# Performance work log

Measured on AMD Instinct MI355X. Metric: run time of the kernel, lower is better.

The kernel has to match this reference:

```python
import jax, jax.numpy as jnp
import numpy as np

EPS = 1e-4      # MovingBatchNorm eps
STEPS = 3       # fixed RK4 steps standing in for adaptive dopri5
B, N, D, C, H = 4, 2048, 3, 64, 512


def setup_inputs() -> dict:
    key = jax.random.key(0)
    ks = iter(jax.random.split(key, 40))
    f32 = jnp.float32

    def rn(shape, s=1.0):
        return jax.random.normal(next(ks), shape, dtype=f32) * s

    inp = {}
    inp['x'] = rn((B, N, D))
    inp['c'] = rn((B, N, C))
    for p in ('bn1', 'bn2'):
        inp[p + '_mean'] = rn((D,), 0.1)
        inp[p + '_var'] = jax.random.uniform(next(ks), (D,), dtype=f32, minval=0.5, maxval=1.5)
        inp[p + '_log_gamma'] = jnp.zeros((D,), f32)
        inp[p + '_beta'] = jnp.zeros((D,), f32)
    inp['sqrt_T'] = jnp.array([np.sqrt(0.5)], f32)  # train_T: T = sqrt_T**2
    dims = [(D, H), (H, H), (H, H), (H, D)]  # concatsquash (in, out)
    for i, (din, dout) in enumerate(dims):
        inp[f'W{i}'] = rn((dout, din), 0.05)
        inp[f'b{i}'] = jnp.zeros((dout,), f32)
        inp[f'Wg{i}'] = rn((dout, C + 1), 0.05)
        inp[f'bg{i}'] = jnp.zeros((dout,), f32)
        inp[f'Wb{i}'] = rn((dout, C + 1), 0.05)
    return inp


def _odenet(t, x, c, layers):
    # ConcatSquash MLP: lin(x)*sigmoid(hyper_gate([t,c])) + hyper_bias([t,c])
    ctx = jnp.concatenate([jnp.broadcast_to(t, c.shape[:-1] + (1,)).astype(x.dtype), c], axis=-1)
    h = x
    for i, (W, b, Wg, bg, Wb) in enumerate(layers):
        h = (h @ W.T + b) * jax.nn.sigmoid(ctx @ Wg.T + bg) + ctx @ Wb.T
        if i < len(layers) - 1:
            h = jnp.tanh(h)
    return h


def _aug_dyn(t, x, c, layers):
    # augmented CNF dynamics: (dx/dt, dlogp/dt) with exact divergence via D jvps
    f = lambda xx: _odenet(t, xx, c, layers)
    div = jnp.zeros(x.shape[:-1] + (1,), x.dtype)
    dx = None
    for i in range(x.shape[-1]):
        e = jnp.zeros_like(x).at[..., i].set(1.0)
        dx, jv = jax.jvp(f, (x,), (e,))
        div = div + jv[..., i:i + 1]
    return dx, -div


def _rk4(x0, lp0, c, layers, T):
    dt = T / STEPS

    def step(carry, i):
        x, lp = carry
        t = i.astype(x.dtype) * dt
        k1x, k1l = _aug_dyn(t, x, c, layers)
        k2x, k2l = _aug_dyn(t + 0.5 * dt, x + 0.5 * dt * k1x, c, layers)
        k3x, k3l = _aug_dyn(t + 0.5 * dt, x + 0.5 * dt * k2x, c, layers)
        k4x, k4l = _aug_dyn(t + dt, x + dt * k3x, c, layers)
        x = x + (dt / 6.0) * (k1x + 2.0 * k2x + 2.0 * k3x + k4x)
        lp = lp + (dt / 6.0) * (k1l + 2.0 * k2l + 2.0 * k3l + k4l)
        return (x, lp), None

    (x, lp), _ = jax.lax.scan(step, (x0, lp0), jnp.arange(STEPS))
    return x, lp


def _bn(x, lp, mean, var, log_gamma, beta):
    # MovingBatchNorm1d, eval mode; logdet = sum(log_gamma - 0.5*log(var+eps))
    y = (x - mean) * jnp.exp(log_gamma) / jnp.sqrt(var + EPS) + beta
    ld = jnp.sum(log_gamma - 0.5 * jnp.log(var + EPS))
    return y, lp - ld


def reference(x, c, bn1_mean, bn1_var, bn1_log_gamma, bn1_beta,
              bn2_mean, bn2_var, bn2_log_gamma, bn2_beta, sqrt_T,
              W0, b0, Wg0, bg0, Wb0, W1, b1, Wg1, bg1, Wb1,
              W2, b2, Wg2, bg2, Wb2, W3, b3, Wg3, bg3, Wb3):
    layers = [(W0, b0, Wg0, bg0, Wb0), (W1, b1, Wg1, bg1, Wb1),
              (W2, b2, Wg2, bg2, Wb2), (W3, b3, Wg3, bg3, Wb3)]
    lp = jnp.zeros(x.shape[:-1] + (1,), x.dtype)  # (B,N,1)
    x, lp = _bn(x, lp, bn1_mean, bn1_var, bn1_log_gamma, bn1_beta)
    T = sqrt_T[0] ** 2
    x, lp = _rk4(x, lp, c, layers, T)
    x, lp = _bn(x, lp, bn2_mean, bn2_var, bn2_log_gamma, bn2_beta)
    return x, jnp.sum(lp, axis=(1, 2))
```

## Files before the change

### kernel.cpp

```cpp
#include <hip/hip_runtime.h>
#include <hip/hip_fp8.h>

#define PTS 8192
#define HDIM 512
#define BN_EPS 1e-4f
#define HSTRB 528
#define TS 256.0f
#define SCL1 0x7f7f7f7f

typedef unsigned short u16;
typedef unsigned char u8;
typedef long long i64;
typedef u16 u16x8 __attribute__((ext_vector_type(8)));
typedef short s16x8 __attribute__((ext_vector_type(8)));
typedef float f32x4 __attribute__((ext_vector_type(4)));
typedef float f32x2 __attribute__((ext_vector_type(2)));
typedef int i32x4 __attribute__((ext_vector_type(4)));
typedef int i32x8 __attribute__((ext_vector_type(8)));

__device__ __forceinline__ float bf2f(u16 u) {
  unsigned x = ((unsigned)u) << 16;
  return __builtin_bit_cast(float, x);
}
__device__ __forceinline__ u16 f2bf(float f) {
  unsigned x = __builtin_bit_cast(unsigned, f);
  x += 0x7fffu + ((x >> 16) & 1u);
  return (u16)(x >> 16);
}
__device__ __forceinline__ u8 f2f8(float x) {
  int v = __builtin_amdgcn_cvt_pk_fp8_f32(x, x, 0, false);
  return (u8)(v & 0xff);
}
__device__ __forceinline__ unsigned pk4_f8(float a, float b, float c, float d) {
  int v = __builtin_amdgcn_cvt_pk_fp8_f32(a, b, 0, false);
  v = __builtin_amdgcn_cvt_pk_fp8_f32(c, d, v, true);
  return (unsigned)v;
}
__device__ __forceinline__ float sigf(float x) {
  return __builtin_amdgcn_rcpf(1.f + __expf(-x));
}
__device__ __forceinline__ float fast_tanh(float x) {
  float e = __expf(2.f * x);
  return 1.f - 2.f * __builtin_amdgcn_rcpf(e + 1.f);
}
__device__ __forceinline__ void gl2lds16(const u16* g, u16* l) {
  __builtin_amdgcn_global_load_lds(
      (const __attribute__((address_space(1))) void*)g,
      (__attribute__((address_space(3))) void*)l, 16, 0, 0);
}
__device__ __forceinline__ i32x8 ld32(const u8* p) {
  i32x4 lo = *(const i32x4*)p;
  i32x4 hi = *(const i32x4*)(p + 16);
  return __builtin_shufflevector(lo, hi, 0, 1, 2, 3, 4, 5, 6, 7);
}

#define MFMA_SC(A, B, C) \
  __builtin_amdgcn_mfma_scale_f32_16x16x128_f8f6f4((A), (B), (C), 0, 0, 0, SCL1, 0, SCL1)

#define MX_GEMM(WL)                                                         \
  {                                                                         \
    _Pragma("unroll")                                                       \
    for (int zi = 0; zi < 4; ++zi)                                          \
      _Pragma("unroll")                                                     \
      for (int zj = 0; zj < 4; ++zj)                                        \
        _Pragma("unroll")                                                   \
        for (int zr = 0; zr < 4; ++zr) acc[zi][zj][zr] = 0.f;               \
    const u8* wp = (WL);                                                    \
    _Pragma("unroll 1")                                                     \
    for (int c = 0; c < 4; ++c) {                                           \
      const u8* hc = hb + c * 128;                                          \
      i32x8 af0 = ld32(hc);                                                 \
      i32x8 af1 = ld32(hc + (size_t)16 * HSTRB);                            \
      i32x8 af2 = ld32(hc + (size_t)32 * HSTRB);                            \
      i32x8 af3 = ld32(hc + (size_t)48 * HSTRB);                            \
      i32x8 bA = ld32(wp);                                                  \
      i32x8 bB = ld32(wp + 2048);                                           \
      __builtin_amdgcn_sched_barrier(0);                                    \
      __builtin_amdgcn_s_setprio(1);                                        \
      acc[0][0] = MFMA_SC(af0, bA, acc[0][0]);                              \
      acc[1][0] = MFMA_SC(af1, bA, acc[1][0]);                              \
      acc[2][0] = MFMA_SC(af2, bA, acc[2][0]);                              \
      acc[3][0] = MFMA_SC(af3, bA, acc[3][0]);                              \
      acc[0][1] = MFMA_SC(af0, bB, acc[0][1]);                              \
      acc[1][1] = MFMA_SC(af1, bB, acc[1][1]);                              \
      acc[2][1] = MFMA_SC(af2, bB, acc[2][1]);                              \
      acc[3][1] = MFMA_SC(af3, bB, acc[3][1]);                              \
      __builtin_amdgcn_s_setprio(0);                                        \
      __builtin_amdgcn_sched_barrier(0);                                    \
      bA = ld32(wp + 4096);                                                 \
      bB = ld32(wp + 6144);                                                 \
      __builtin_amdgcn_sched_barrier(0);                                    \
      __builtin_amdgcn_s_setprio(1);                                        \
      acc[0][2] = MFMA_SC(af0, bA, acc[0][2]);                              \
      acc[1][2] = MFMA_SC(af1, bA, acc[1][2]);                              \
      acc[2][2] = MFMA_SC(af2, bA, acc[2][2]);                              \
      acc[3][2] = MFMA_SC(af3, bA, acc[3][2]);                              \
      acc[0][3] = MFMA_SC(af0, bB, acc[0][3]);                              \
      acc[1][3] = MFMA_SC(af1, bB, acc[1][3]);                              \
      acc[2][3] = MFMA_SC(af2, bB, acc[2][3]);                              \
      acc[3][3] = MFMA_SC(af3, bB, acc[3][3]);                              \
      __builtin_amdgcn_s_setprio(0);                                        \
      __builtin_amdgcn_sched_barrier(0);                                    \
      wp += 65536;                                                          \
    }                                                                       \
  }

struct PrepArgs {
  const float *W1, *W2;
  u8 *W1s, *W2s;
  const float* c;
  u16* cb;
  const float *Wg0, *Wg1, *Wg2, *Wb0, *Wb1, *Wb2;
  const float *bg0, *bg1, *bg2;
  u16* Wpack;
  float* bias_pack;
  const float *x, *m1, *v1, *lg1, *be1;
  float *x_cur;
  const float *Wg3, *bg3, *Wb3;
  float *G3, *B3;
  const float *W0, *b0, *b1, *b2, *W3;
  float *E0, *E1, *E2;
};
__global__ void prep_kernel(PrepArgs a) {
  int i = blockIdx.x * 256 + threadIdx.x;
  if (i < 512 * 512) {
    int n = i >> 9, k = i & 511;
    int c = k >> 7, q2 = (k >> 5) & 3, b = k & 31;
    int w = n >> 6, j = (n >> 4) & 3, lr = n & 15;
    size_t d = (size_t)c * 65536 + (size_t)w * 8192 + (size_t)j * 2048 +
               (size_t)(q2 * 16 + lr) * 32 + b;
    a.W1s[d] = f2f8(a.W1[i]);
    a.W2s[d] = f2f8(a.W2[i]);
  }
  if (i < PTS * 64) a.cb[i] = f2bf(a.c[i]);
  if (i < 6 * 512 * 64) {
    int sec = i >> 15;
    int within = i & 32767;
    int o = within >> 6, k = within & 63;
    const float* src[6] = {a.Wg0, a.Wg1, a.Wg2, a.Wb0, a.Wb1, a.Wb2};
    a.Wpack[i] = f2bf(src[sec][o * 65 + 1 + k]);
  }
  if (i < 3072) {
    int sec = i >> 9, o = i & 511;
    const float* bgl[3] = {a.bg0, a.bg1, a.bg2};
    a.bias_pack[i] = (sec < 3) ? bgl[sec][o] : 0.f;
  }
  if (i < 512) {
    int o = i;
    a.E0[o * 8 + 0] = a.W0[o * 3];
    a.E0[o * 8 + 1] = a.W0[o * 3 + 1];
    a.E0[o * 8 + 2] = a.W0[o * 3 + 2];
    a.E0[o * 8 + 3] = a.b0[o];
    a.E0[o * 8 + 4] = a.Wg0[o * 65];
    a.E0[o * 8 + 5] = a.Wb0[o * 65];
    a.E0[o * 8 + 6] = 0.f; a.E0[o * 8 + 7] = 0.f;
    a.E1[o * 4 + 0] = a.b1[o];
    a.E1[o * 4 + 1] = a.Wg1[o * 65];
    a.E1[o * 4 + 2] = a.Wb1[o * 65];
    a.E1[o * 4 + 3] = 0.f;
    a.E2[o * 8 + 0] = a.b2[o];
    a.E2[o * 8 + 1] = a.Wg2[o * 65];
    a.E2[o * 8 + 2] = a.Wb2[o * 65];
    a.E2[o * 8 + 3] = a.W3[o];
    a.E2[o * 8 + 4] = a.W3[512 + o];
    a.E2[o * 8 + 5] = a.W3[1024 + o];
    a.E2[o * 8 + 6] = 0.f; a.E2[o * 8 + 7] = 0.f;
  }
  if (i < PTS * 3) {
    int d = i % 3;
    a.x_cur[i] = (a.x[i] - a.m1[d]) * __expf(a.lg1[d]) * rsqrtf(a.v1[d] + BN_EPS) + a.be1[d];
  }
  {
    int lane = threadIdx.x & 63;
    int p = (blockIdx.x * 256 + threadIdx.x) >> 6;
    float cv = a.c[(size_t)p * 64 + lane];
    float ag[3], ab[3];
    #pragma unroll
    for (int o = 0; o < 3; ++o) {
      ag[o] = cv * a.Wg3[o * 65 + 1 + lane];
      ab[o] = cv * a.Wb3[o * 65 + 1 + lane];
    }
    #pragma unroll
    for (int off = 32; off > 0; off >>= 1) {
      #pragma unroll
      for (int o = 0; o < 3; ++o) {
        ag[o] += __shfl_xor(ag[o], off);
        ab[o] += __shfl_xor(ab[o], off);
      }
    }
    if (lane == 0) {
      #pragma unroll
      for (int o = 0; o < 3; ++o) {
        a.G3[p * 3 + o] = ag[o] + a.bg3[o];
        a.B3[p * 3 + o] = ab[o];
      }
    }
  }
}

struct GatesGemmArgs {
  const u16 *A, *W;
  const float* bias;
  u16* GBi;
};
__global__ __launch_bounds__(256) void gates_gemm(GatesGemmArgs a) {
  __shared__ u16 As[128 * 32];
  __shared__ u16 Bs[128 * 32];
  int tid = threadIdx.x;
  int m0 = blockIdx.x * 128, n0 = blockIdx.y * 128;
  int wave = tid >> 6, lane = tid & 63;
  int wm = (wave & 1) * 64, wn = (wave >> 1) * 64;
  int lr = lane & 15, quad = lane >> 4;

  int rowS = tid >> 2, colS = (tid & 3) * 8;
  const u16* gA0 = a.A + (size_t)(m0 + rowS) * 64 + colS;
  const u16* gB0 = a.W + (size_t)(n0 + rowS) * 64 + colS;
  u16* sA0 = &As[tid * 8];
  u16* sA1 = &As[2048 + tid * 8];
  u16* sB0 = &Bs[tid * 8];
  u16* sB1 = &Bs[2048 + tid * 8];

  f32x4 acc[4][4];
  #pragma unroll
  for (int i = 0; i < 4; ++i)
    #pragma unroll
    for (int j = 0; j < 4; ++j)
      #pragma unroll
      for (int r = 0; r < 4; ++r) acc[i][j][r] = 0.f;

  for (int k0 = 0; k0 < 64; k0 += 32) {
    if (k0) __syncthreads();
    gl2lds16(gA0 + k0, sA0);
    gl2lds16(gA0 + (size_t)64 * 64 + k0, sA1);
    gl2lds16(gB0 + k0, sB0);
    gl2lds16(gB0 + (size_t)64 * 64 + k0, sB1);
    __syncthreads();
    s16x8 af[4], bfr[4];
    #pragma unroll
    for (int i = 0; i < 4; ++i)
      af[i] = *(const s16x8*)&As[(wm + i * 16 + lr) * 32 + quad * 8];
    #pragma unroll
    for (int j = 0; j < 4; ++j)
      bfr[j] = *(const s16x8*)&Bs[(wn + j * 16 + lr) * 32 + quad * 8];
    #pragma unroll
    for (int i = 0; i < 4; ++i)
      #pragma unroll
      for (int j = 0; j < 4; ++j)
        acc[i][j] = __builtin_amdgcn_mfma_f32_16x16x32_bf16(af[i], bfr[j], acc[i][j], 0, 0, 0);
  }

  #pragma unroll
  for (int j = 0; j < 4; ++j) {
    int n = n0 + wn + j * 16 + lr;
    int sec = n >> 9, col = n & 511;
    int l = (sec < 3) ? sec : sec - 3;
    int off = col * 2 + ((sec < 3) ? 0 : 1);
    float bv = a.bias[n];
    u16* outp = a.GBi + (size_t)l * PTS * 1024 + off;
    #pragma unroll
    for (int i = 0; i < 4; ++i) {
      int mrow = m0 + wm + i * 16 + quad * 4;
      #pragma unroll
      for (int r = 0; r < 4; ++r)
        outp[(size_t)(mrow + r) * 1024] = f2bf(acc[i][j][r] + bv);
    }
  }
}

struct FlowArgs {
  const float* sqrtT;
  const float *G3, *B3, *Wg3, *Wb3, *b3;
  const float* x0;
  const u16 *GBi0, *GBi1, *GBi2;
  const float *E0, *E1, *E2;
  const u8 *W1s, *W2s;
  const float *m2, *v2, *lg2, *be2;
  float* out_x;
  float* lp_state;
};

__global__ __launch_bounds__(512, 4) void flow_kernel(FlowArgs a) {
  __shared__ __align__(16) u8 Hs[64 * HSTRB];
  __shared__ float xe[16][3];
  __shared__ float part[8][16][6];
  __shared__ float xs[16][3], kxs[16][3];
  __shared__ float kls[16], lps[16];
  __shared__ float g3s[16][3], b3s[16][3];

  int tid = threadIdx.x;
  int w = tid >> 6, lane = tid & 63, lr = lane & 15, quad = lane >> 4;
  int n0 = w * 64;
  int p0 = blockIdx.x * 16;
  float s0 = a.sqrtT[0];
  float dt = s0 * s0 * (1.f / 3.f);

  const u8* w1l = a.W1s + (size_t)w * 8192 + (size_t)lane * 32;
  const u8* w2l = a.W2s + (size_t)w * 8192 + (size_t)lane * 32;
  const u8* hb = (const u8*)Hs + (size_t)lr * HSTRB + quad * 32;

  float wg3r[3], wb3r[3], b3r[3];
  #pragma unroll
  for (int r = 0; r < 3; ++r) {
    wg3r[r] = a.Wg3[r * 65];
    wb3r[r] = a.Wb3[r * 65];
    b3r[r] = a.b3[r];
  }

  if (tid < 16) {
    int p = p0 + tid;
    #pragma unroll
    for (int r = 0; r < 3; ++r) {
      xs[tid][r] = a.x0[p * 3 + r];
      g3s[tid][r] = a.G3[p * 3 + r];
      b3s[tid][r] = a.B3[p * 3 + r];
    }
    lps[tid] = 0.f;
  }

  int pl0 = tid >> 5;
  int base_o = (tid & 31) * 16;
  const u16* g0row = a.GBi0 + (size_t)(p0 + pl0) * 1024 + 2 * base_o;

  #pragma unroll 1
  for (int s = 0; s < 12; ++s) {
    int sub = s & 3;
    float ts_cur = (float)(s >> 2) + ((sub == 0) ? 0.f : (sub == 3) ? 1.f : 0.5f);

    u16x8 gc0 = *(const u16x8*)(g0row);
    u16x8 gc1 = *(const u16x8*)(g0row + 8);
    u16x8 gc2 = *(const u16x8*)(g0row + 16);
    u16x8 gc3 = *(const u16x8*)(g0row + 24);

    __syncthreads();

    if (tid < 16) {
      float o0 = xs[tid][0], o1 = xs[tid][1], o2 = xs[tid][2];
      if (s > 0) {
        int m = (s - 1) & 3;
        float ts_prev = (float)((s - 1) >> 2) + ((m == 0) ? 0.f : (m == 3) ? 1.f : 0.5f);
        float tp = ts_prev * dt;
        float fr[6];
        #pragma unroll
        for (int r = 0; r < 6; ++r) {
          float sum = part[0][tid][r];
          #pragma unroll
          for (int ww = 1; ww < 8; ++ww) sum += part[ww][tid][r];
          fr[r] = sum;
        }
        float dx[3], gate[3];
        #pragma unroll
        for (int r = 0; r < 3; ++r) {
          gate[r] = sigf(g3s[tid][r] + tp * wg3r[r]);
          float bias = b3s[tid][r] + tp * wb3r[r];
          dx[r] = fmaf(fr[r] + b3r[r], gate[r], bias);
        }
        float klv = -(fr[3] * gate[0] + fr[4] * gate[1] + fr[5] * gate[2]);
        if (m == 0) {
          o0 += 0.5f * dt * dx[0]; o1 += 0.5f * dt * dx[1]; o2 += 0.5f * dt * dx[2];
          kxs[tid][0] = dx[0]; kxs[tid][1] = dx[1]; kxs[tid][2] = dx[2];
          kls[tid] = klv;
        } else if (m == 1) {
          o0 += 0.5f * dt * dx[0]; o1 += 0.5f * dt * dx[1]; o2 += 0.5f * dt * dx[2];
          kxs[tid][0] += 2.f * dx[0]; kxs[tid][1] += 2.f * dx[1]; kxs[tid][2] += 2.f * dx[2];
          kls[tid] += 2.f * klv;
        } else if (m == 2) {
          o0 += dt * dx[0]; o1 += dt * dx[1]; o2 += dt * dx[2];
          kxs[tid][0] += 2.f * dx[0]; kxs[tid][1] += 2.f * dx[1]; kxs[tid][2] += 2.f * dx[2];
          kls[tid] += 2.f * klv;
        } else {
          float sc = dt * (1.f / 6.f);
          o0 = xs[tid][0] + sc * (kxs[tid][0] + dx[0]);
          o1 = xs[tid][1] + sc * (kxs[tid][1] + dx[1]);
          o2 = xs[tid][2] + sc * (kxs[tid][2] + dx[2]);
          xs[tid][0] = o0; xs[tid][1] = o1; xs[tid][2] = o2;
          lps[tid] += sc * (kls[tid] + klv);
        }
      }
      xe[tid][0] = o0; xe[tid][1] = o1; xe[tid][2] = o2;
    }
    __syncthreads();

    float t = ts_cur * dt;

    {
      float x0v = xe[pl0][0], x1v = xe[pl0][1], x2v = xe[pl0][2];
      u16x8 gcv[4] = {gc0, gc1, gc2, gc3};
      #pragma unroll
      for (int cc = 0; cc < 4; ++cc) {
        u16x8 v = gcv[cc];
        float hk[4], d0k[4], d1k[4], d2k[4];
        #pragma unroll
        for (int k = 0; k < 4; ++k) {
          int o = base_o + cc * 4 + k;
          f32x4 e = *(const f32x4*)(a.E0 + (size_t)o * 8);
          f32x2 e2 = *(const f32x2*)(a.E0 + (size_t)o * 8 + 4);
          float u = fmaf(e[0], x0v, fmaf(e[1], x1v, e[2] * x2v)) + e[3];
          float gate = sigf(bf2f(v[2 * k]) + t * e2[0]);
          float bias = bf2f(v[2 * k + 1]) + t * e2[1];
          float z = fmaf(u, gate, bias);
          float h = fast_tanh(z);
          float wm = (1.f - h * h) * gate * TS;
          hk[k] = h;
          d0k[k] = wm * e[0];
          d1k[k] = wm * e[1];
          d2k[k] = wm * e[2];
        }
        size_t hbb = (size_t)(pl0 * 4) * HSTRB + base_o + cc * 4;
        *(unsigned*)(Hs + hbb) = pk4_f8(hk[0], hk[1], hk[2], hk[3]);
        *(unsigned*)(Hs + hbb + HSTRB) = pk4_f8(d0k[0], d0k[1], d0k[2], d0k[3]);
        *(unsigned*)(Hs + hbb + 2 * HSTRB) = pk4_f8(d1k[0], d1k[1], d1k[2], d1k[3]);
        *(unsigned*)(Hs + hbb + 3 * HSTRB) = pk4_f8(d2k[0], d2k[1], d2k[2], d2k[3]);
      }
    }
    __syncthreads();

    f32x4 acc[4][4];
    MX_GEMM(w1l)

    unsigned g1v[4][4];
    #pragma unroll
    for (int j = 0; j < 4; ++j)
      #pragma unroll
      for (int i = 0; i < 4; ++i)
        g1v[j][i] = *(const unsigned*)(a.GBi1 + (size_t)(p0 + i * 4 + quad) * 1024 +
                                       2 * (n0 + j * 16 + lr));

    __syncthreads();

    #pragma unroll
    for (int j = 0; j < 4; ++j) {
      int n = n0 + j * 16 + lr;
      f32x4 e1 = *(const f32x4*)(a.E1 + (size_t)n * 4);
      #pragma unroll
      for (int i = 0; i < 4; ++i) {
        unsigned d = g1v[j][i];
        float gate = sigf(bf2f((u16)(d & 0xffffu)) + t * e1[1]);
        float bias = bf2f((u16)(d >> 16)) + t * e1[2];
        f32x4 u = acc[i][j];
        float z = fmaf(u[0] + e1[0], gate, bias);
        float h = fast_tanh(z);
        float wmf = (1.f - h * h) * gate;
        int row = i * 16 + quad * 4;
        Hs[(size_t)row * HSTRB + n] = f2f8(h);
        Hs[(size_t)(row + 1) * HSTRB + n] = f2f8(u[1] * wmf);
        Hs[(size_t)(row + 2) * HSTRB + n] = f2f8(u[2] * wmf);
        Hs[(size_t)(row + 3) * HSTRB + n] = f2f8(u[3] * wmf);
      }
    }
    __syncthreads();

    MX_GEMM(w2l)

    unsigned g2v[4][4];
    #pragma unroll
    for (int j = 0; j < 4; ++j)
      #pragma unroll
      for (int i = 0; i < 4; ++i)
        g2v[j][i] = *(const unsigned*)(a.GBi2 + (size_t)(p0 + i * 4 + quad) * 1024 +
                                       2 * (n0 + j * 16 + lr));

    #pragma unroll
    for (int i = 0; i < 4; ++i) {
      float v0 = 0.f, v1 = 0.f, v2 = 0.f, v3 = 0.f, v4 = 0.f, v5 = 0.f;
      int pl = i * 4 + quad;
      #pragma unroll
      for (int j = 0; j < 4; ++j) {
        int n = n0 + j * 16 + lr;
        f32x4 ea = *(const f32x4*)(a.E2 + (size_t)n * 8);
        f32x2 eb = *(const f32x2*)(a.E2 + (size_t)n * 8 + 4);
        unsigned d = g2v[j][i];
        float gate = sigf(bf2f((u16)(d & 0xffffu)) + t * ea[1]);
        float bias = bf2f((u16)(d >> 16)) + t * ea[2];
        f32x4 u = acc[i][j];
        float z = fmaf(u[0] + ea[0], gate, bias);
        float h = fast_tanh(z);
        float wmf = (1.f - h * h) * gate;
        float w30 = ea[3], w31 = eb[0], w32 = eb[1];
        v0 = fmaf(h, w30, v0);
        v1 = fmaf(h, w31, v1);
        v2 = fmaf(h, w32, v2);
        v3 = fmaf(u[1] * wmf, w30, v3);
        v4 = fmaf(u[2] * wmf, w31, v4);
        v5 = fmaf(u[3] * wmf, w32, v5);
      }
      #pragma unroll
      for (int mask = 1; mask <= 8; mask <<= 1) {
        v0 += __shfl_xor(v0, mask);
        v1 += __shfl_xor(v1, mask);
        v2 += __shfl_xor(v2, mask);
        v3 += __shfl_xor(v3, mask);
        v4 += __shfl_xor(v4, mask);
        v5 += __shfl_xor(v5, mask);
      }
      float val = (lr == 0) ? v0 : (lr == 1) ? v1 : (lr == 2) ? v2
                : (lr == 3) ? v3 * (1.f / TS) : (lr == 4) ? v4 * (1.f / TS)
                : v5 * (1.f / TS);
      if (lr < 6) part[w][pl][lr] = val;
    }
  }

  __syncthreads();

  if (tid < 16) {
    int p = p0 + tid;
    float tp = 3.f * dt;
    float fr[6];
    #pragma unroll
    for (int r = 0; r < 6; ++r) {
      float sum = part[0][tid][r];
      #pragma unroll
      for (int ww = 1; ww < 8; ++ww) sum += part[ww][tid][r];
      fr[r] = sum;
    }
    float dx[3], gate[3];
    #pragma unroll
    for (int r = 0; r < 3; ++r) {
      gate[r] = sigf(g3s[tid][r] + tp * wg3r[r]);
      float bias = b3s[tid][r] + tp * wb3r[r];
      dx[r] = fmaf(fr[r] + b3r[r], gate[r], bias);
    }
    float klv = -(fr[3] * gate[0] + fr[4] * gate[1] + fr[5] * gate[2]);
    float sc = dt * (1.f / 6.f);
    #pragma unroll
    for (int r = 0; r < 3; ++r) {
      float xf = xs[tid][r] + sc * (kxs[tid][r] + dx[r]);
      a.out_x[p * 3 + r] =
          (xf - a.m2[r]) * __expf(a.lg2[r]) * rsqrtf(a.v2[r] + BN_EPS) + a.be2[r];
    }
    a.lp_state[p] = lps[tid] + sc * (kls[tid] + klv);
  }
}

__global__ void finish_lp(const float* __restrict__ lp_state,
                          const float* __restrict__ v1, const float* __restrict__ lg1,
                          const float* __restrict__ v2, const float* __restrict__ lg2,
                          float* __restrict__ out) {
  int b = blockIdx.x, tid = threadIdx.x;
  float s = 0.f;
  for (int n = tid; n < 2048; n += 256) s += lp_state[b * 2048 + n];
  __shared__ float red[256];
  red[tid] = s;
  __syncthreads();
  for (int w = 128; w > 0; w >>= 1) {
    if (tid < w) red[tid] += red[tid + w];
    __syncthreads();
  }
  if (tid == 0) {
    float ld = 0.f;
    for (int d = 0; d < 3; ++d) {
      ld += lg1[d] - 0.5f * logf(v1[d] + BN_EPS);
      ld += lg2[d] - 0.5f * logf(v2[d] + BN_EPS);
    }
    out[b] = red[0] - 2048.f * ld;
  }
}

extern "C" void kernel_launch(void* const* d_in, const int* in_sizes, int n_in,
                              void* d_out, int out_size, void* d_ws, size_t ws_size,
                              hipStream_t stream) {
  const float* x        = (const float*)d_in[0];
  const float* c        = (const float*)d_in[1];
  const float* bn1_mean = (const float*)d_in[2];
  const float* bn1_var  = (const float*)d_in[3];
  const float* bn1_lg   = (const float*)d_in[4];
  const float* bn1_beta = (const float*)d_in[5];
  const float* bn2_mean = (const float*)d_in[6];
  const float* bn2_var  = (const float*)d_in[7];
  const float* bn2_lg   = (const float*)d_in[8];
  const float* bn2_beta = (const float*)d_in[9];
  const float* sqrtT    = (const float*)d_in[10];
  const float* W0  = (const float*)d_in[11];
  const float* b0  = (const float*)d_in[12];
  const float* Wg0 = (const float*)d_in[13];
  const float* bg0 = (const float*)d_in[14];
  const float* Wb0 = (const float*)d_in[15];
  const float* W1  = (const float*)d_in[16];
  const float* b1  = (const float*)d_in[17];
  const float* Wg1 = (const float*)d_in[18];
  const float* bg1 = (const float*)d_in[19];
  const float* Wb1 = (const float*)d_in[20];
  const float* W2  = (const float*)d_in[21];
  const float* b2  = (const float*)d_in[22];
  const float* Wg2 = (const float*)d_in[23];
  const float* bg2 = (const float*)d_in[24];
  const float* Wb2 = (const float*)d_in[25];
  const float* W3  = (const float*)d_in[26];
  const float* b3  = (const float*)d_in[27];
  const float* Wg3 = (const float*)d_in[28];
  const float* bg3 = (const float*)d_in[29];
  const float* Wb3 = (const float*)d_in[30];

  char* base = (char*)d_ws;
  size_t off = 0;
  auto alloc = [&](size_t bytes) -> void* {
    void* pp = base + off;
    off += (bytes + 255) & ~(size_t)255;
    return pp;
  };
  u8* W1s = (u8*)alloc((size_t)512 * 512);
  u8* W2s = (u8*)alloc((size_t)512 * 512);
  u16* cb  = (u16*)alloc((size_t)PTS * 64 * 2);
  u16* Wpack = (u16*)alloc((size_t)6 * 512 * 64 * 2);
  float* bias_pack = (float*)alloc((size_t)3072 * 4);
  u16* GBi = (u16*)alloc((size_t)3 * PTS * 1024 * 2);
  const size_t SZi = (size_t)PTS * 1024;
  u16* GBi0 = GBi;
  u16* GBi1 = GBi + SZi;
  u16* GBi2 = GBi + 2 * SZi;
  float* G3f = (float*)alloc((size_t)PTS * 3 * 4);
  float* B3f = (float*)alloc((size_t)PTS * 3 * 4);
  float* E0 = (float*)alloc((size_t)512 * 8 * 4);
  float* E1 = (float*)alloc((size_t)512 * 4 * 4);
  float* E2 = (float*)alloc((size_t)512 * 8 * 4);
  float* x_cur    = (float*)alloc((size_t)PTS * 3 * 4);
  float* lp_state = (float*)alloc((size_t)PTS * 4);
  (void)ws_size; (void)in_sizes; (void)n_in; (void)out_size;

  PrepArgs pa{W1, W2, W1s, W2s, c, cb, Wg0, Wg1, Wg2, Wb0, Wb1, Wb2,
              bg0, bg1, bg2, Wpack, bias_pack, x, bn1_mean, bn1_var,
              bn1_lg, bn1_beta, x_cur, Wg3, bg3, Wb3, G3f, B3f,
              W0, b0, b1, b2, W3, E0, E1, E2};
  prep_kernel<<<2048, 256, 0, stream>>>(pa);

  GatesGemmArgs gg{cb, Wpack, bias_pack, GBi};
  gates_gemm<<<dim3(64, 24), 256, 0, stream>>>(gg);

  FlowArgs fa{sqrtT, G3f, B3f, Wg3, Wb3, b3, x_cur, GBi0, GBi1, GBi2,
              E0, E1, E2, W1s, W2s, bn2_mean, bn2_var, bn2_lg, bn2_beta,
              (float*)d_out, lp_state};
  flow_kernel<<<PTS / 16, 512, 0, stream>>>(fa);

  finish_lp<<<4, 256, 0, stream>>>(lp_state, bn1_var, bn1_lg, bn2_var, bn2_lg,
                                   (float*)d_out + PTS * 3);
}
```

Baseline: 563.8 us.

## Double-buffer hidden LDS and compute RK state redundantly to drop barriers

Splits the shared hidden-activation buffer into two (one per GEMM layer), so the barrier between the first GEMM and the layer-2 activation writes can be removed. The per-substep RK4 state update, previously done by 16 threads and broadcast through shared memory behind an extra barrier, is now recomputed by every thread for its own point. Only one designated thread per point writes the shared state, and the x state is double-buffered by step parity. It also prefetches next-substep layer-0 gate/bias loads and hoists pointer arithmetic for the gate loads. This trades more LDS and redundant ALU work for two fewer block-wide barriers per substep.

```diff
diff --git a/kernel.cpp b/kernel.cpp
--- a/kernel.cpp
+++ b/kernel.cpp
@@ -57,7 +57,7 @@
 #define MFMA_SC(A, B, C) \
   __builtin_amdgcn_mfma_scale_f32_16x16x128_f8f6f4((A), (B), (C), 0, 0, 0, SCL1, 0, SCL1)
 
-#define MX_GEMM(WL)                                                         \
+#define MX_GEMM(WL, HB)                                                     \
   {                                                                         \
     _Pragma("unroll")                                                       \
     for (int zi = 0; zi < 4; ++zi)                                          \
@@ -68,7 +68,7 @@
     const u8* wp = (WL);                                                    \
     _Pragma("unroll 1")                                                     \
     for (int c = 0; c < 4; ++c) {                                           \
-      const u8* hc = hb + c * 128;                                          \
+      const u8* hc = (HB) + c * 128;                                        \
       i32x8 af0 = ld32(hc);                                                 \
       i32x8 af1 = ld32(hc + (size_t)16 * HSTRB);                            \
       i32x8 af2 = ld32(hc + (size_t)32 * HSTRB);                            \
@@ -280,10 +280,10 @@
 };
 
 __global__ __launch_bounds__(512, 4) void flow_kernel(FlowArgs a) {
-  __shared__ __align__(16) u8 Hs[64 * HSTRB];
-  __shared__ float xe[16][3];
-  __shared__ float part[8][16][6];
-  __shared__ float xs[16][3], kxs[16][3];
+  __shared__ __align__(16) u8 HsA[64 * HSTRB];
+  __shared__ __align__(16) u8 HsB[64 * HSTRB];
+  __shared__ float part[8][16][8];
+  __shared__ float xs[2][16][3], kxs[16][3];
   __shared__ float kls[16], lps[16];
   __shared__ float g3s[16][3], b3s[16][3];
 
@@ -291,12 +291,16 @@
   int w = tid >> 6, lane = tid & 63, lr = lane & 15, quad = lane >> 4;
   int n0 = w * 64;
   int p0 = blockIdx.x * 16;
+  int pl0 = tid >> 5;
+  int base_o = (tid & 31) * 16;
+  bool desig = (tid & 31) == 0;
   float s0 = a.sqrtT[0];
   float dt = s0 * s0 * (1.f / 3.f);
 
   const u8* w1l = a.W1s + (size_t)w * 8192 + (size_t)lane * 32;
   const u8* w2l = a.W2s + (size_t)w * 8192 + (size_t)lane * 32;
-  const u8* hb = (const u8*)Hs + (size_t)lr * HSTRB + quad * 32;
+  const u8* hbA = (const u8*)HsA + (size_t)lr * HSTRB + quad * 32;
+  const u8* hbB = (const u8*)HsB + (size_t)lr * HSTRB + quad * 32;
 
   float wg3r[3], wb3r[3], b3r[3];
   #pragma unroll
@@ -306,84 +310,83 @@
     b3r[r] = a.b3[r];
   }
 
-  if (tid < 16) {
-    int p = p0 + tid;
+  const u16* g0p = a.GBi0 + (size_t)(p0 + pl0) * 1024 + 2 * base_o;
+  const u16* g1p = a.GBi1 + (size_t)(p0 + quad) * 1024 + 2 * (n0 + lr);
+  const u16* g2p = a.GBi2 + (size_t)(p0 + quad) * 1024 + 2 * (n0 + lr);
+
+  if (desig) {
     #pragma unroll
     for (int r = 0; r < 3; ++r) {
-      xs[tid][r] = a.x0[p * 3 + r];
-      g3s[tid][r] = a.G3[p * 3 + r];
-      b3s[tid][r] = a.B3[p * 3 + r];
-    }
-    lps[tid] = 0.f;
-  }
-
-  int pl0 = tid >> 5;
-  int base_o = (tid & 31) * 16;
-  const u16* g0row = a.GBi0 + (size_t)(p0 + pl0) * 1024 + 2 * base_o;
+      xs[0][pl0][r] = a.x0[(p0 + pl0) * 3 + r];
+      g3s[pl0][r] = a.G3[(p0 + pl0) * 3 + r];
+      b3s[pl0][r] = a.B3[(p0 + pl0) * 3 + r];
+    }
+    lps[pl0] = 0.f;
+  }
+  u16x8 gc0 = *(const u16x8*)(g0p);
+  u16x8 gc1 = *(const u16x8*)(g0p + 8);
+  u16x8 gc2 = *(const u16x8*)(g0p + 16);
+  u16x8 gc3 = *(const u16x8*)(g0p + 24);
+  __syncthreads();
 
   #pragma unroll 1
   for (int s = 0; s < 12; ++s) {
     int sub = s & 3;
-    float ts_cur = (float)(s >> 2) + ((sub == 0) ? 0.f : (sub == 3) ? 1.f : 0.5f);
-
-    u16x8 gc0 = *(const u16x8*)(g0row);
-    u16x8 gc1 = *(const u16x8*)(g0row + 8);
-    u16x8 gc2 = *(const u16x8*)(g0row + 16);
-    u16x8 gc3 = *(const u16x8*)(g0row + 24);
-
-    __syncthreads();
-
-    if (tid < 16) {
-      float o0 = xs[tid][0], o1 = xs[tid][1], o2 = xs[tid][2];
-      if (s > 0) {
-        int m = (s - 1) & 3;
-        float ts_prev = (float)((s - 1) >> 2) + ((m == 0) ? 0.f : (m == 3) ? 1.f : 0.5f);
-        float tp = ts_prev * dt;
-        float fr[6];
-        #pragma unroll
-        for (int r = 0; r < 6; ++r) {
-          float sum = part[0][tid][r];
-          #pragma unroll
-          for (int ww = 1; ww < 8; ++ww) sum += part[ww][tid][r];
-          fr[r] = sum;
+    float t = ((float)(s >> 2) + ((sub == 0) ? 0.f : (sub == 3) ? 1.f : 0.5f)) * dt;
+
+    float o0, o1, o2;
+    if (s == 0) {
+      o0 = xs[0][pl0][0]; o1 = xs[0][pl0][1]; o2 = xs[0][pl0][2];
+    } else {
+      int m = (s - 1) & 3, q = (s - 1) >> 2;
+      float tp = ((float)q + ((m == 0) ? 0.f : (m == 3) ? 1.f : 0.5f)) * dt;
+      float fr0 = 0.f, fr1 = 0.f, fr2 = 0.f, fr3 = 0.f, fr4 = 0.f, fr5 = 0.f;
+      #pragma unroll
+      for (int ww = 0; ww < 8; ++ww) {
+        f32x4 pa = *(const f32x4*)&part[ww][pl0][0];
+        f32x2 pb = *(const f32x2*)&part[ww][pl0][4];
+        fr0 += pa[0]; fr1 += pa[1]; fr2 += pa[2];
+        fr3 += pa[3]; fr4 += pb[0]; fr5 += pb[1];
+      }
+      float ga0 = sigf(g3s[pl0][0] + tp * wg3r[0]);
+      float ga1 = sigf(g3s[pl0][1] + tp * wg3r[1]);
+      float ga2 = sigf(g3s[pl0][2] + tp * wg3r[2]);
+      float dx0 = fmaf(fr0 + b3r[0], ga0, b3s[pl0][0] + tp * wb3r[0]);
+      float dx1 = fmaf(fr1 + b3r[1], ga1, b3s[pl0][1] + tp * wb3r[1]);
+      float dx2 = fmaf(fr2 + b3r[2], ga2, b3s[pl0][2] + tp * wb3r[2]);
+      float klv = -(fr3 * ga0 + fr4 * ga1 + fr5 * ga2);
+      float bx0 = xs[q & 1][pl0][0];
+      float bx1 = xs[q & 1][pl0][1];
+      float bx2 = xs[q & 1][pl0][2];
+      if (m == 3) {
+        float sc = dt * (1.f / 6.f);
+        o0 = bx0 + sc * (kxs[pl0][0] + dx0);
+        o1 = bx1 + sc * (kxs[pl0][1] + dx1);
+        o2 = bx2 + sc * (kxs[pl0][2] + dx2);
+        if (desig) {
+          xs[(q + 1) & 1][pl0][0] = o0;
+          xs[(q + 1) & 1][pl0][1] = o1;
+          xs[(q + 1) & 1][pl0][2] = o2;
+          lps[pl0] += sc * (kls[pl0] + klv);
         }
-        float dx[3], gate[3];
-        #pragma unroll
-        for (int r = 0; r < 3; ++r) {
-          gate[r] = sigf(g3s[tid][r] + tp * wg3r[r]);
-          float bias = b3s[tid][r] + tp * wb3r[r];
-          dx[r] = fmaf(fr[r] + b3r[r], gate[r], bias);
+      } else {
+        float cf = (m == 2) ? dt : 0.5f * dt;
+        o0 = fmaf(cf, dx0, bx0);
+        o1 = fmaf(cf, dx1, bx1);
+        o2 = fmaf(cf, dx2, bx2);
+        if (desig) {
+          if (m == 0) {
+            kxs[pl0][0] = dx0; kxs[pl0][1] = dx1; kxs[pl0][2] = dx2;
+            kls[pl0] = klv;
+          } else {
+            kxs[pl0][0] += 2.f * dx0; kxs[pl0][1] += 2.f * dx1; kxs[pl0][2] += 2.f * dx2;
+            kls[pl0] += 2.f * klv;
+          }
         }
-        float klv = -(fr[3] * gate[0] + fr[4] * gate[1] + fr[5] * gate[2]);
-        if (m == 0) {
-          o0 += 0.5f * dt * dx[0]; o1 += 0.5f * dt * dx[1]; o2 += 0.5f * dt * dx[2];
-          kxs[tid][0] = dx[0]; kxs[tid][1] = dx[1]; kxs[tid][2] = dx[2];
-          kls[tid] = klv;
-        } else if (m == 1) {
-          o0 += 0.5f * dt * dx[0]; o1 += 0.5f * dt * dx[1]; o2 += 0.5f * dt * dx[2];
-          kxs[tid][0] += 2.f * dx[0]; kxs[tid][1] += 2.f * dx[1]; kxs[tid][2] += 2.f * dx[2];
-          kls[tid] += 2.f * klv;
-        } else if (m == 2) {
-          o0 += dt * dx[0]; o1 += dt * dx[1]; o2 += dt * dx[2];
-          kxs[tid][0] += 2.f * dx[0]; kxs[tid][1] += 2.f * dx[1]; kxs[tid][2] += 2.f * dx[2];
-          kls[tid] += 2.f * klv;
-        } else {
-          float sc = dt * (1.f / 6.f);
-          o0 = xs[tid][0] + sc * (kxs[tid][0] + dx[0]);
-          o1 = xs[tid][1] + sc * (kxs[tid][1] + dx[1]);
-          o2 = xs[tid][2] + sc * (kxs[tid][2] + dx[2]);
-          xs[tid][0] = o0; xs[tid][1] = o1; xs[tid][2] = o2;
-          lps[tid] += sc * (kls[tid] + klv);
-        }
-      }
-      xe[tid][0] = o0; xe[tid][1] = o1; xe[tid][2] = o2;
-    }
-    __syncthreads();
-
-    float t = ts_cur * dt;
+      }
+    }
 
     {
-      float x0v = xe[pl0][0], x1v = xe[pl0][1], x2v = xe[pl0][2];
       u16x8 gcv[4] = {gc0, gc1, gc2, gc3};
       #pragma unroll
       for (int cc = 0; cc < 4; ++cc) {
@@ -394,7 +397,7 @@
           int o = base_o + cc * 4 + k;
           f32x4 e = *(const f32x4*)(a.E0 + (size_t)o * 8);
           f32x2 e2 = *(const f32x2*)(a.E0 + (size_t)o * 8 + 4);
-          float u = fmaf(e[0], x0v, fmaf(e[1], x1v, e[2] * x2v)) + e[3];
+          float u = fmaf(e[0], o0, fmaf(e[1], o1, e[2] * o2)) + e[3];
           float gate = sigf(bf2f(v[2 * k]) + t * e2[0]);
           float bias = bf2f(v[2 * k + 1]) + t * e2[1];
           float z = fmaf(u, gate, bias);
@@ -406,26 +409,24 @@
           d2k[k] = wm * e[2];
         }
         size_t hbb = (size_t)(pl0 * 4) * HSTRB + base_o + cc * 4;
-        *(unsigned*)(Hs + hbb) = pk4_f8(hk[0], hk[1], hk[2], hk[3]);
-        *(unsigned*)(Hs + hbb + HSTRB) = pk4_f8(d0k[0], d0k[1], d0k[2], d0k[3]);
-        *(unsigned*)(Hs + hbb + 2 * HSTRB) = pk4_f8(d1k[0], d1k[1], d1k[2], d1k[3]);
-        *(unsigned*)(Hs + hbb + 3 * HSTRB) = pk4_f8(d2k[0], d2k[1], d2k[2], d2k[3]);
+        *(unsigned*)(HsA + hbb) = pk4_f8(hk[0], hk[1], hk[2], hk[3]);
+        *(unsigned*)(HsA + hbb + HSTRB) = pk4_f8(d0k[0], d0k[1], d0k[2], d0k[3]);
+        *(unsigned*)(HsA + hbb + 2 * HSTRB) = pk4_f8(d1k[0], d1k[1], d1k[2], d1k[3]);
+        *(unsigned*)(HsA + hbb + 3 * HSTRB) = pk4_f8(d2k[0], d2k[1], d2k[2], d2k[3]);
       }
     }
     __syncthreads();
 
     f32x4 acc[4][4];
-    MX_GEMM(w1l)
-
+    MX_GEMM(w1l, hbA)
+
+    asm("" : "+v"(g1p));
     unsigned g1v[4][4];
     #pragma unroll
     for (int j = 0; j < 4; ++j)
       #pragma unroll
       for (int i = 0; i < 4; ++i)
-        g1v[j][i] = *(const unsigned*)(a.GBi1 + (size_t)(p0 + i * 4 + quad) * 1024 +
-                                       2 * (n0 + j * 16 + lr));
-
-    __syncthreads();
+        g1v[j][i] = *(const unsigned*)(g1p + (size_t)i * 4096 + j * 32);
 
     #pragma unroll
     for (int j = 0; j < 4; ++j) {
@@ -441,23 +442,29 @@
         float h = fast_tanh(z);
         float wmf = (1.f - h * h) * gate;
         int row = i * 16 + quad * 4;
-        Hs[(size_t)row * HSTRB + n] = f2f8(h);
-        Hs[(size_t)(row + 1) * HSTRB + n] = f2f8(u[1] * wmf);
-        Hs[(size_t)(row + 2) * HSTRB + n] = f2f8(u[2] * wmf);
-        Hs[(size_t)(row + 3) * HSTRB + n] = f2f8(u[3] * wmf);
+        HsB[(size_t)row * HSTRB + n] = f2f8(h);
+        HsB[(size_t)(row + 1) * HSTRB + n] = f2f8(u[1] * wmf);
+        HsB[(size_t)(row + 2) * HSTRB + n] = f2f8(u[2] * wmf);
+        HsB[(size_t)(row + 3) * HSTRB + n] = f2f8(u[3] * wmf);
       }
     }
     __syncthreads();
 
-    MX_GEMM(w2l)
-
+    MX_GEMM(w2l, hbB)
+
+    asm("" : "+v"(g2p));
     unsigned g2v[4][4];
     #pragma unroll
     for (int j = 0; j < 4; ++j)
       #pragma unroll
       for (int i = 0; i < 4; ++i)
-        g2v[j][i] = *(const unsigned*)(a.GBi2 + (size_t)(p0 + i * 4 + quad) * 1024 +
-                                       2 * (n0 + j * 16 + lr));
+        g2v[j][i] = *(const unsigned*)(g2p + (size_t)i * 4096 + j * 32);
+
+    asm("" : "+v"(g0p));
+    gc0 = *(const u16x8*)(g0p);
+    gc1 = *(const u16x8*)(g0p + 8);
+    gc2 = *(const u16x8*)(g0p + 16);
+    gc3 = *(const u16x8*)(g0p + 24);
 
     #pragma unroll
     for (int i = 0; i < 4; ++i) {
@@ -497,37 +504,36 @@
                 : v5 * (1.f / TS);
       if (lr < 6) part[w][pl][lr] = val;
     }
-  }
-
-  __syncthreads();
-
-  if (tid < 16) {
-    int p = p0 + tid;
+    __syncthreads();
+  }
+
+  if (desig) {
+    int p = p0 + pl0;
     float tp = 3.f * dt;
-    float fr[6];
-    #pragma unroll
-    for (int r = 0; r < 6; ++r) {
-      float sum = part[0][tid][r];
-      #pragma unroll
-      for (int ww = 1; ww < 8; ++ww) sum += part[ww][tid][r];
-      fr[r] = sum;
-    }
-    float dx[3], gate[3];
+    float fr0 = 0.f, fr1 = 0.f, fr2 = 0.f, fr3 = 0.f, fr4 = 0.f, fr5 = 0.f;
+    #pragma unroll
+    for (int ww = 0; ww < 8; ++ww) {
+      f32x4 pa = *(const f32x4*)&part[ww][pl0][0];
+      f32x2 pb = *(const f32x2*)&part[ww][pl0][4];
+      fr0 += pa[0]; fr1 += pa[1]; fr2 += pa[2];
+      fr3 += pa[3]; fr4 += pb[0]; fr5 += pb[1];
+    }
+    float ga0 = sigf(g3s[pl0][0] + tp * wg3r[0]);
+    float ga1 = sigf(g3s[pl0][1] + tp * wg3r[1]);
+    float ga2 = sigf(g3s[pl0][2] + tp * wg3r[2]);
+    float dx[3];
+    dx[0] = fmaf(fr0 + b3r[0], ga0, b3s[pl0][0] + tp * wb3r[0]);
+    dx[1] = fmaf(fr1 + b3r[1], ga1, b3s[pl0][1] + tp * wb3r[1]);
+    dx[2] = fmaf(fr2 + b3r[2], ga2, b3s[pl0][2] + tp * wb3r[2]);
+    float klv = -(fr3 * ga0 + fr4 * ga1 + fr5 * ga2);
+    float sc = dt * (1.f / 6.f);
     #pragma unroll
     for (int r = 0; r < 3; ++r) {
-      gate[r] = sigf(g3s[tid][r] + tp * wg3r[r]);
-      float bias = b3s[tid][r] + tp * wb3r[r];
-      dx[r] = fmaf(fr[r] + b3r[r], gate[r], bias);
-    }
-    float klv = -(fr[3] * gate[0] + fr[4] * gate[1] + fr[5] * gate[2]);
-    float sc = dt * (1.f / 6.f);
-    #pragma unroll
-    for (int r = 0; r < 3; ++r) {
-      float xf = xs[tid][r] + sc * (kxs[tid][r] + dx[r]);
+      float xf = xs[0][pl0][r] + sc * (kxs[pl0][r] + dx[r]);
       a.out_x[p * 3 + r] =
           (xf - a.m2[r]) * __expf(a.lg2[r]) * rsqrtf(a.v2[r] + BN_EPS) + a.be2[r];
     }
-    a.lp_state[p] = lps[tid] + sc * (kls[tid] + klv);
+    a.lp_state[p] = lps[pl0] + sc * (kls[pl0] + klv);
   }
 }
 
```

New measurement: 530.7 us, median of 2. -5.9%, faster.
